# Kernel tuning notes

Hardware: AMD Instinct MI355X
Metric: run time of the kernel (lower is better)

## Reference

```python
import jax, jax.numpy as jnp
import numpy as np

N = 4096        # total nodes per batched graph
E_EDGES = 65536 # edges per graph (avg degree 16)
B = 16          # graphs in batch
NFEAT = 1280
NHID = 512
NHEAD = 8
DFF = 2048      # TransformerEncoderLayer default dim_feedforward
HD = NHID // NHEAD
LN_EPS = 1e-5


def setup_inputs() -> dict:
    key = jax.random.key(0)
    ks = jax.random.split(key, 32)
    s = 0.02
    inp = {}
    inp["fea1"] = jax.random.normal(ks[0], (N, NFEAT), jnp.float32)
    inp["fea2"] = jax.random.normal(ks[1], (N, NFEAT), jnp.float32)
    inp["src1"] = jax.random.randint(ks[2], (E_EDGES,), 0, N, jnp.int32)
    inp["dst1"] = jax.random.randint(ks[3], (E_EDGES,), 0, N, jnp.int32)
    inp["src2"] = jax.random.randint(ks[4], (E_EDGES,), 0, N, jnp.int32)
    inp["dst2"] = jax.random.randint(ks[5], (E_EDGES,), 0, N, jnp.int32)
    seg = ((jnp.arange(N) * B) // N).astype(jnp.int32)  # equal-size graphs, sorted ids
    inp["seg1"] = seg
    inp["seg2"] = seg
    inp["num_graphs"] = B
    # GraphConv params (torch Linear convention: y = x @ W.T + b)
    inp["W1"] = jax.random.normal(ks[6], (NHID, NFEAT), jnp.float32) * s
    inp["b1"] = jnp.zeros((NHID,), jnp.float32)
    inp["W2"] = jax.random.normal(ks[7], (NHID, NHID), jnp.float32) * s
    inp["b2"] = jnp.zeros((NHID,), jnp.float32)
    # TransformerEncoderLayer params
    inp["in_proj_w"] = jax.random.normal(ks[8], (3 * NHID, NHID), jnp.float32) * s
    inp["in_proj_b"] = jnp.zeros((3 * NHID,), jnp.float32)
    inp["out_proj_w"] = jax.random.normal(ks[9], (NHID, NHID), jnp.float32) * s
    inp["out_proj_b"] = jnp.zeros((NHID,), jnp.float32)
    inp["ln1_g"] = jnp.ones((NHID,), jnp.float32)
    inp["ln1_b"] = jnp.zeros((NHID,), jnp.float32)
    inp["ln2_g"] = jnp.ones((NHID,), jnp.float32)
    inp["ln2_b"] = jnp.zeros((NHID,), jnp.float32)
    inp["ff1_w"] = jax.random.normal(ks[10], (DFF, NHID), jnp.float32) * s
    inp["ff1_b"] = jnp.zeros((DFF,), jnp.float32)
    inp["ff2_w"] = jax.random.normal(ks[11], (NHID, DFF), jnp.float32) * s
    inp["ff2_b"] = jnp.zeros((NHID,), jnp.float32)
    # MLP head
    inp["l1_w"] = jax.random.normal(ks[12], (512, NHID), jnp.float32) * s
    inp["l1_b"] = jnp.zeros((512,), jnp.float32)
    inp["l2_w"] = jax.random.normal(ks[13], (128, 512), jnp.float32) * s
    inp["l2_b"] = jnp.zeros((128,), jnp.float32)
    inp["l3_w"] = jax.random.normal(ks[14], (2, 128), jnp.float32) * s
    inp["l3_b"] = jnp.zeros((2,), jnp.float32)
    return inp


def graph_conv(fea, src, dst, W, b):
    # DGL GraphConv, norm='both': D_in^{-1/2} A D_out^{-1/2} X W + b (W applied pre-agg)
    ones = jnp.ones(src.shape[0], fea.dtype)
    deg_out = jnp.maximum(jax.ops.segment_sum(ones, src, num_segments=N), 1.0)
    deg_in = jnp.maximum(jax.ops.segment_sum(ones, dst, num_segments=N), 1.0)
    h = fea * (deg_out ** -0.5)[:, None]
    h = h @ W.T  # [N, nhid]
    agg = jax.ops.segment_sum(h[src], dst, num_segments=N)  # scatter-add over edges
    return agg * (deg_in ** -0.5)[:, None] + b


def layer_norm(x, g, b):
    mu = jnp.mean(x, -1, keepdims=True)
    var = jnp.mean((x - mu) ** 2, -1, keepdims=True)
    return (x - mu) * jax.lax.rsqrt(var + LN_EPS) * g + b


def encoder_layer(x, in_proj_w, in_proj_b, out_proj_w, out_proj_b,
                  ln1_g, ln1_b, ln2_g, ln2_b, ff1_w, ff1_b, ff2_w, ff2_b):
    # post-norm TransformerEncoderLayer, unbatched [S, E] input, eval mode (no dropout)
    qkv = x @ in_proj_w.T + in_proj_b               # [S, 3E]
    q, k, v = jnp.split(qkv, 3, axis=-1)
    S = x.shape[0]
    q = q.reshape(S, NHEAD, HD).transpose(1, 0, 2)  # [H, S, hd]
    k = k.reshape(S, NHEAD, HD).transpose(1, 0, 2)
    v = v.reshape(S, NHEAD, HD).transpose(1, 0, 2)
    scores = jnp.einsum('hqd,hkd->hqk', q, k) / jnp.sqrt(jnp.float32(HD))
    attn = jax.nn.softmax(scores, axis=-1)
    ctx = jnp.einsum('hqk,hkd->hqd', attn, v).transpose(1, 0, 2).reshape(S, NHID)
    x = layer_norm(x + (ctx @ out_proj_w.T + out_proj_b), ln1_g, ln1_b)
    ff = jax.nn.relu(x @ ff1_w.T + ff1_b) @ ff2_w.T + ff2_b
    return layer_norm(x + ff, ln2_g, ln2_b)


def mean_nodes(fea, seg, num_graphs):
    counts = jnp.maximum(jax.ops.segment_sum(jnp.ones(fea.shape[0], fea.dtype), seg, num_segments=num_graphs), 1.0)
    return jax.ops.segment_sum(fea, seg, num_segments=num_graphs) / counts[:, None]


def reference(fea1, fea2, W1, b1, W2, b2, in_proj_w, in_proj_b, out_proj_w, out_proj_b,
              ln1_g, ln1_b, ln2_g, ln2_b, ff1_w, ff1_b, ff2_w, ff2_b,
              l1_w, l1_b, l2_w, l2_b, l3_w, l3_b,
              src1, dst1, src2, dst2, seg1, seg2, num_graphs):
    tparams = (in_proj_w, in_proj_b, out_proj_w, out_proj_b,
               ln1_g, ln1_b, ln2_g, ln2_b, ff1_w, ff1_b, ff2_w, ff2_b)
    h1 = jax.nn.relu(graph_conv(fea1, src1, dst1, W1, b1))
    h2 = jax.nn.relu(graph_conv(fea2, src2, dst2, W1, b1))
    h1 = encoder_layer(h1, *tparams)
    h2 = encoder_layer(h2, *tparams)
    h1 = jax.nn.relu(graph_conv(h1, src1, dst1, W2, b2))
    h2 = jax.nn.relu(graph_conv(h2, src2, dst2, W2, b2))
    hg = mean_nodes(h1, seg1, num_graphs) * mean_nodes(h2, seg2, num_graphs)  # [B, nhid]
    out = hg @ l1_w.T + l1_b          # note: original has NO activation between l1/l2/l3
    out = out @ l2_w.T + l2_b
    return jax.nn.softmax(out @ l3_w.T + l3_b, axis=-1)
```

## Files before the change

kernel.cpp:

```cpp
#include <hip/hip_runtime.h>
#include <hip/hip_bf16.h>
#include <math.h>

#define NN 4096
#define EE 65536
#define NS 8192
#define NFEAT 1280
#define NHID 512
#define DFF 2048

typedef unsigned short u16;
typedef unsigned int u32;
typedef __attribute__((ext_vector_type(8))) short bf16x8;
typedef __attribute__((ext_vector_type(4))) float f32x4;
#define MFMA16(A,B,C) __builtin_amdgcn_mfma_f32_16x16x32_bf16(A,B,C,0,0,0)
#define GAS __attribute__((address_space(1)))
#define LAS __attribute__((address_space(3)))

#define SCL 0.18033688011112042f
#define THR 11.541560327111707f

static const size_t OFF_A   = 0ull;
static const size_t OFF_HP  = 8388608ull;
static const size_t OFF_X   = 12582912ull;
static const size_t OFF_XB  = 16777216ull;
static const size_t OFF_E   = 18874368ull;
static const size_t OFF_VT  = 25165824ull;
static const size_t OFF_CTB = 27262976ull;
static const size_t OFF_W1B = 29360128ull;
static const size_t OFF_IPB = 29687808ull;
static const size_t OFF_OPB = 30081024ull;
static const size_t OFF_F1B = 30212096ull;
static const size_t OFF_F2B = 30736384ull;
static const size_t OFF_W2B = 31260672ull;
static const size_t OFF_ME  = 31391744ull;
static const size_t OFF_DG  = 31408128ull;
static const size_t OFF_INT = 31424512ull;

#define IH_S1 0
#define IH_D1 4096
#define IH_S2 8192
#define IH_D2 12288
#define IO_F1 16384
#define IO_F2 20608
#define IC_1  24832
#define IC_2  28928
#define IE_1  33024
#define IE_2  98560

__device__ __forceinline__ u16 f2b(float x) {
    u32 u = __float_as_uint(x);
    return (u16)((u + 0x7fffu + ((u >> 16) & 1u)) >> 16);
}
__device__ __forceinline__ float b_lo(u32 u) { return __uint_as_float(u << 16); }
__device__ __forceinline__ float b_hi(u32 u) { return __uint_as_float(u & 0xffff0000u); }

__global__ __launch_bounds__(256) void k_hist(const int* __restrict__ s1, const int* __restrict__ d1,
                                              const int* __restrict__ s2, const int* __restrict__ d2,
                                              int* __restrict__ I)
{
    int e = blockIdx.x * 256 + threadIdx.x;
    if (e < EE) {
        atomicAdd(&I[IH_S1 + s1[e]], 1);
        atomicAdd(&I[IH_D1 + d1[e]], 1);
        atomicAdd(&I[IH_S2 + s2[e]], 1);
        atomicAdd(&I[IH_D2 + d2[e]], 1);
    }
}

__global__ __launch_bounds__(256) void k_deg_fin(const int* __restrict__ I, float* __restrict__ deg)
{
    int i = blockIdx.x * 256 + threadIdx.x;
    if (i < 4 * NN) deg[i] = rsqrtf(fmaxf((float)I[i], 1.0f));
}

__global__ __launch_bounds__(256) void k_scan(int* __restrict__ I)
{
    int b = blockIdx.x;
    const int* hist = I + (b ? IH_D2 : IH_D1);
    int* offs = I + (b ? IO_F2 : IO_F1);
    int* cur  = I + (b ? IC_2 : IC_1);
    __shared__ int part[256];
    int t = threadIdx.x;
    int base = t * 16;
    int loc[16];
    int s = 0;
#pragma unroll
    for (int i = 0; i < 16; ++i) { loc[i] = s; s += hist[base + i]; }
    part[t] = s;
    __syncthreads();
    if (t == 0) {
        int a = 0;
        for (int i = 0; i < 256; ++i) { int v = part[i]; part[i] = a; a += v; }
        offs[NN] = a;
    }
    __syncthreads();
    int p = part[t];
#pragma unroll
    for (int i = 0; i < 16; ++i) { offs[base + i] = p + loc[i]; cur[base + i] = p + loc[i]; }
}

__global__ __launch_bounds__(256) void k_fill(const int* __restrict__ s1, const int* __restrict__ d1,
                                              const int* __restrict__ s2, const int* __restrict__ d2,
                                              int* __restrict__ I)
{
    int e = blockIdx.x * 256 + threadIdx.x;
    if (e < EE) {
        int p1 = atomicAdd(&I[IC_1 + d1[e]], 1);
        I[IE_1 + p1] = s1[e];
        int p2 = atomicAdd(&I[IC_2 + d2[e]], 1);
        I[IE_2 + p2] = s2[e];
    }
}

__global__ __launch_bounds__(256) void k_cvt(const float* __restrict__ src, u16* __restrict__ dst, int n)
{
    int i = (blockIdx.x * 256 + threadIdx.x) * 8;
    if (i >= n) return;
    float4 a = *(const float4*)&src[i];
    float4 b = *(const float4*)&src[i + 4];
    uint4 o;
    o.x = (u32)f2b(a.x) | ((u32)f2b(a.y) << 16);
    o.y = (u32)f2b(a.z) | ((u32)f2b(a.w) << 16);
    o.z = (u32)f2b(b.x) | ((u32)f2b(b.y) << 16);
    o.w = (u32)f2b(b.z) | ((u32)f2b(b.w) << 16);
    *(uint4*)&dst[i] = o;
}

__global__ __launch_bounds__(256) void k_scale_bf(const float* __restrict__ in1, const float* __restrict__ in2,
                                                  const float* __restrict__ sc1, const float* __restrict__ sc2,
                                                  u16* __restrict__ out, int ncol)
{
    int quads = ncol >> 2;
    long long idx = (long long)blockIdx.x * 256 + threadIdx.x;
    if (idx >= (long long)NS * quads) return;
    int r  = (int)(idx / quads);
    int cq = (int)(idx % quads) * 4;
    const float* in; const float* sc; int rr;
    if (r < NN) { in = in1; sc = sc1; rr = r; } else { in = in2; sc = sc2; rr = r - NN; }
    float4 v = *(const float4*)&in[(size_t)rr * ncol + cq];
    float s = sc[rr];
    uint2 o;
    o.x = (u32)f2b(v.x * s) | ((u32)f2b(v.y * s) << 16);
    o.y = (u32)f2b(v.z * s) | ((u32)f2b(v.w * s) << 16);
    *(uint2*)&out[(size_t)r * ncol + cq] = o;
}

template<int BN>
__global__ __launch_bounds__(256) void k_gemm_bf(const u16* __restrict__ A, const u16* __restrict__ W,
                                                 const float* __restrict__ bias, float* __restrict__ Cf,
                                                 u16* __restrict__ Cb, int M, int N, int K, int relu)
{
    constexpr int RM = (BN == 128) ? 4 : 2;
    __shared__ u16 As[128 * 32];
    __shared__ u16 Bs[BN * 32];
    int t = threadIdx.x;
    int w = t >> 6, L = t & 63;
    int lm = L & 15, lq = L >> 4;
    int wr = (BN == 128) ? (w >> 1) : w;
    int wc = (BN == 128) ? (w & 1) : 0;
    int row0 = blockIdx.y * 128, col0 = blockIdx.x * BN;
    f32x4 acc[RM][4];
#pragma unroll
    for (int i = 0; i < RM; ++i)
#pragma unroll
        for (int j = 0; j < 4; ++j) acc[i][j] = (f32x4){0.f, 0.f, 0.f, 0.f};

    const u16* As0 = &A[(size_t)(row0 + (w * 2) * 16 + (L >> 2)) * K + (L & 3) * 8];
    const u16* As1 = As0 + (size_t)16 * K;
    const u16* Bs0 = &W[(size_t)(col0 + ((BN == 128) ? (w * 2) * 16 : w * 16) + (L >> 2)) * K + (L & 3) * 8];
    const u16* Bs1 = Bs0 + (size_t)16 * K;
    u16* AsW = &As[(w * 2) * 512];
    u16* BsW = (BN == 128) ? &Bs[(w * 2) * 512] : &Bs[w * 512];

    for (int k0 = 0; k0 < K; k0 += 32) {
        if (k0) __syncthreads();
        __builtin_amdgcn_global_load_lds((const GAS void*)(As0 + k0), (LAS void*)(LAS char*)AsW, 16, 0, 0);
        __builtin_amdgcn_global_load_lds((const GAS void*)(As1 + k0), (LAS void*)((LAS char*)AsW + 1024), 16, 0, 0);
        __builtin_amdgcn_global_load_lds((const GAS void*)(Bs0 + k0), (LAS void*)(LAS char*)BsW, 16, 0, 0);
        if constexpr (BN == 128)
            __builtin_amdgcn_global_load_lds((const GAS void*)(Bs1 + k0), (LAS void*)((LAS char*)BsW + 1024), 16, 0, 0);
        __syncthreads();
        bf16x8 af[RM], bw[4];
#pragma unroll
        for (int i = 0; i < RM; ++i)
            af[i] = *(const bf16x8*)&As[(wr * (RM * 16) + i * 16 + lm) * 32 + lq * 8];
#pragma unroll
        for (int j = 0; j < 4; ++j)
            bw[j] = *(const bf16x8*)&Bs[(wc * 64 + j * 16 + lm) * 32 + lq * 8];
#pragma unroll
        for (int i = 0; i < RM; ++i)
#pragma unroll
            for (int j = 0; j < 4; ++j)
                acc[i][j] = MFMA16(af[i], bw[j], acc[i][j]);
    }

#pragma unroll
    for (int i = 0; i < RM; ++i) {
        int row = row0 + wr * (RM * 16) + i * 16 + lq * 4;
#pragma unroll
        for (int j = 0; j < 4; ++j) {
            int col = col0 + wc * 64 + j * 16 + lm;
            float bv = bias ? bias[col] : 0.0f;
#pragma unroll
            for (int r = 0; r < 4; ++r) {
                float v = acc[i][j][r] + bv;
                if (relu) v = fmaxf(v, 0.0f);
                size_t off = (size_t)(row + r) * N + col;
                if (Cb) Cb[off] = f2b(v);
                else    Cf[off] = v;
            }
        }
    }
}

__global__ __launch_bounds__(256) void k_gather_bf(const u16* __restrict__ hp, const int* __restrict__ I,
                                                   const float* __restrict__ din1, const float* __restrict__ din2,
                                                   const float* __restrict__ bias,
                                                   float* __restrict__ xout, u16* __restrict__ xb)
{
    int r = blockIdx.x, c = threadIdx.x;
    int g = r >> 12, rl = r & (NN - 1);
    const int* off = I + (g ? IO_F2 : IO_F1);
    const int* eid = I + (g ? IE_2 : IE_1);
    int beg = off[rl], end = off[rl + 1];
    const u16* base = hp + ((size_t)g << 12) * NHID;
    float a0 = 0.f, a1 = 0.f;
    for (int i = beg; i < end; ++i) {
        u32 v = ((const u32*)(base + (size_t)eid[i] * NHID))[c];
        a0 += b_lo(v);
        a1 += b_hi(v);
    }
    float s = (g ? din2 : din1)[rl];
    float2 bv = *(const float2*)&bias[c * 2];
    float v0 = fmaxf(fmaf(a0, s, bv.x), 0.f);
    float v1 = fmaxf(fmaf(a1, s, bv.y), 0.f);
    size_t o = (size_t)r * NHID + c * 2;
    if (xout) *(float2*)&xout[o] = make_float2(v0, v1);
    if (xb) *(u32*)&xb[o] = (u32)f2b(v0) | ((u32)f2b(v1) << 16);
}

__global__ __launch_bounds__(256) void k_vtrans(const u16* __restrict__ qkvb, u16* __restrict__ vtb)
{
    __shared__ u16 tile[64][65];
    int t = threadIdx.x;
    int kt = blockIdx.x, h = blockIdx.y, g = blockIdx.z;
    int k0 = kt * 64;
    size_t gbase = (size_t)g * NN;
#pragma unroll
    for (int p = 0; p < 4; ++p) {
        int kl = p * 16 + (t >> 4);
        int d  = (t & 15) * 4;
        uint2 v = *(const uint2*)&qkvb[(gbase + k0 + kl) * 1536 + 1024 + h * 64 + d];
        tile[kl][d + 0] = (u16)(v.x & 0xffff);
        tile[kl][d + 1] = (u16)(v.x >> 16);
        tile[kl][d + 2] = (u16)(v.y & 0xffff);
        tile[kl][d + 3] = (u16)(v.y >> 16);
    }
    __syncthreads();
#pragma unroll
    for (int p = 0; p < 4; ++p) {
        int dl = p * 16 + (t >> 4);
        int kap = (t & 15) * 4;
        u16 v0 = tile[(t & 15) + 0][dl];
        u16 v1 = tile[(t & 15) + 16][dl];
        u16 v2 = tile[(t & 15) + 32][dl];
        u16 v3 = tile[(t & 15) + 48][dl];
        uint2 o;
        o.x = (u32)v0 | ((u32)v1 << 16);
        o.y = (u32)v2 | ((u32)v3 << 16);
        *(uint2*)&vtb[((size_t)(g * 8 + h) * 64 + dl) * (size_t)NN + k0 + kap] = o;
    }
}

__global__ __launch_bounds__(256, 2) void k_attn(const u16* __restrict__ qkv,
                                                 const u16* __restrict__ vt,
                                                 u16* __restrict__ ctb)
{
    __shared__ __align__(16) u16 Kl[2][64 * 64];
    __shared__ __align__(16) u16 Vl[2][64 * 64];
    __shared__ __align__(16) u16 Pl[4][32 * 64];
    int t = threadIdx.x;
    int w = t >> 6, L = t & 63;
    int lm = L & 15, lq = L >> 4;
    int qt = blockIdx.x, h = blockIdx.y, g = blockIdx.z;
    size_t gbase = (size_t)g * NN;
    int q0 = qt * 128 + w * 32;

    const u16* kbase = &qkv[gbase * 1536 + 512 + h * 64];
    const u16* vbase = &vt[(size_t)(g * 8 + h) * 64 * (size_t)NN];

    int srcb = ((L & 7) * 16) ^ ((L >> 3) << 4);
    int rho0 = (w * 2) * 8 + (L >> 3);
    int rho1 = rho0 + 8;
    int kp0 = (rho0 & 15) * 4 + (rho0 >> 4);
    int kp1 = (rho1 & 15) * 4 + (rho1 >> 4);
    const u16* kg0 = &kbase[(size_t)kp0 * 1536 + (srcb >> 1)];
    const u16* kg1 = &kbase[(size_t)kp1 * 1536 + (srcb >> 1)];
    const u16* vg0 = &vbase[(size_t)rho0 * NN + (srcb >> 1)];
    const u16* vg1 = &vbase[(size_t)rho1 * NN + (srcb >> 1)];
    u16* Pw = &Pl[w][0];

    bf16x8 qa[2][2];
#pragma unroll
    for (int qg = 0; qg < 2; ++qg) {
        const u16* qp = &qkv[(gbase + q0 + qg * 16 + lm) * 1536 + h * 64 + lq * 8];
        qa[qg][0] = *(const bf16x8*)qp;
        qa[qg][1] = *(const bf16x8*)(qp + 32);
    }
    f32x4 ctx[2][4];
#pragma unroll
    for (int qg = 0; qg < 2; ++qg)
#pragma unroll
        for (int n = 0; n < 4; ++n) ctx[qg][n] = (f32x4){0.f, 0.f, 0.f, 0.f};
    float m[2][4], lsum[2][4];
#pragma unroll
    for (int qg = 0; qg < 2; ++qg)
#pragma unroll
        for (int r = 0; r < 4; ++r) { m[qg][r] = -1e30f; lsum[qg][r] = 0.0f; }

    __builtin_amdgcn_global_load_lds((const GAS void*)kg0, (LAS void*)((LAS char*)&Kl[0][0] + (w * 2) * 1024), 16, 0, 0);
    __builtin_amdgcn_global_load_lds((const GAS void*)kg1, (LAS void*)((LAS char*)&Kl[0][0] + (w * 2 + 1) * 1024), 16, 0, 0);
    __builtin_amdgcn_global_load_lds((const GAS void*)vg0, (LAS void*)((LAS char*)&Vl[0][0] + (w * 2) * 1024), 16, 0, 0);
    __builtin_amdgcn_global_load_lds((const GAS void*)vg1, (LAS void*)((LAS char*)&Vl[0][0] + (w * 2 + 1) * 1024), 16, 0, 0);
    __syncthreads();

    int cur = 0;
    for (int t0 = 0; t0 < NN; t0 += 64) {
        if (t0 + 64 < NN) {
            size_t ko = (size_t)(t0 + 64) * 1536;
            __builtin_amdgcn_global_load_lds((const GAS void*)(kg0 + ko), (LAS void*)((LAS char*)&Kl[cur ^ 1][0] + (w * 2) * 1024), 16, 0, 0);
            __builtin_amdgcn_global_load_lds((const GAS void*)(kg1 + ko), (LAS void*)((LAS char*)&Kl[cur ^ 1][0] + (w * 2 + 1) * 1024), 16, 0, 0);
            __builtin_amdgcn_global_load_lds((const GAS void*)(vg0 + t0 + 64), (LAS void*)((LAS char*)&Vl[cur ^ 1][0] + (w * 2) * 1024), 16, 0, 0);
            __builtin_amdgcn_global_load_lds((const GAS void*)(vg1 + t0 + 64), (LAS void*)((LAS char*)&Vl[cur ^ 1][0] + (w * 2 + 1) * 1024), 16, 0, 0);
        }
        const char* Kc = (const char*)&Kl[cur][0];
        const char* Vc = (const char*)&Vl[cur][0];
        int sw = (lm & 7) << 4;

        f32x4 s[2][4];
        __builtin_amdgcn_s_setprio(1);
#pragma unroll
        for (int kc = 0; kc < 4; ++kc) {
            const char* rp = Kc + (kc * 16 + lm) * 128;
            bf16x8 kb0 = *(const bf16x8*)(rp + ((lq * 16) ^ sw));
            bf16x8 kb1 = *(const bf16x8*)(rp + ((64 + lq * 16) ^ sw));
#pragma unroll
            for (int qg = 0; qg < 2; ++qg) {
                f32x4 z = (f32x4){0.f, 0.f, 0.f, 0.f};
                z = MFMA16(qa[qg][0], kb0, z);
                z = MFMA16(qa[qg][1], kb1, z);
                s[qg][kc] = z * SCL;
            }
        }
        __builtin_amdgcn_s_setprio(0);

        float dmax = -1e30f;
#pragma unroll
        for (int qg = 0; qg < 2; ++qg)
#pragma unroll
            for (int r = 0; r < 4; ++r) {
                float a = fmaxf(fmaxf(s[qg][0][r], s[qg][1][r]), fmaxf(s[qg][2][r], s[qg][3][r]));
                dmax = fmaxf(dmax, a - m[qg][r]);
            }
        if (__any(dmax > THR)) {
#pragma unroll
            for (int qg = 0; qg < 2; ++qg)
#pragma unroll
                for (int r = 0; r < 4; ++r) {
                    float mr = fmaxf(fmaxf(s[qg][0][r], s[qg][1][r]), fmaxf(s[qg][2][r], s[qg][3][r]));
                    mr = fmaxf(mr, __shfl_xor(mr, 1));
                    mr = fmaxf(mr, __shfl_xor(mr, 2));
                    mr = fmaxf(mr, __shfl_xor(mr, 4));
                    mr = fmaxf(mr, __shfl_xor(mr, 8));
                    float mn = fmaxf(m[qg][r], mr);
                    float corr = exp2f(m[qg][r] - mn);
                    m[qg][r] = mn;
                    lsum[qg][r] *= corr;
#pragma unroll
                    for (int n = 0; n < 4; ++n) ctx[qg][n][r] *= corr;
                }
        }
#pragma unroll
        for (int qg = 0; qg < 2; ++qg)
#pragma unroll
            for (int r = 0; r < 4; ++r) {
                float mq = m[qg][r];
                float p0 = exp2f(s[qg][0][r] - mq);
                float p1 = exp2f(s[qg][1][r] - mq);
                float p2 = exp2f(s[qg][2][r] - mq);
                float p3 = exp2f(s[qg][3][r] - mq);
                lsum[qg][r] += (p0 + p1) + (p2 + p3);
                int row = qg * 16 + lq * 4 + r;
                __hip_bfloat162 c0 = __float22bfloat162_rn(make_float2(p0, p1));
                __hip_bfloat162 c1 = __float22bfloat162_rn(make_float2(p2, p3));
                uint2 pv;
                pv.x = *(u32*)&c0;
                pv.y = *(u32*)&c1;
                *(uint2*)((char*)Pw + row * 128 + ((lm * 8) ^ ((row & 7) << 4))) = pv;
            }

        __builtin_amdgcn_s_setprio(1);
        bf16x8 vbf[4][2];
#pragma unroll
        for (int n = 0; n < 4; ++n) {
            const char* vr = Vc + (n * 16 + lm) * 128;
            vbf[n][0] = *(const bf16x8*)(vr + ((lq * 16) ^ sw));
            vbf[n][1] = *(const bf16x8*)(vr + ((64 + lq * 16) ^ sw));
        }
#pragma unroll
        for (int qg = 0; qg < 2; ++qg) {
            const char* pr = (const char*)Pw + (qg * 16 + lm) * 128;
            bf16x8 pa0 = *(const bf16x8*)(pr + ((lq * 16) ^ sw));
            bf16x8 pa1 = *(const bf16x8*)(pr + ((64 + lq * 16) ^ sw));
#pragma unroll
            for (int n = 0; n < 4; ++n) {
                ctx[qg][n] = MFMA16(pa0, vbf[n][0], ctx[qg][n]);
                ctx[qg][n] = MFMA16(pa1, vbf[n][1], ctx[qg][n]);
            }
        }
        __builtin_amdgcn_s_setprio(0);

        __syncthreads();
        cur ^= 1;
    }

#pragma unroll
    for (int qg = 0; qg < 2; ++qg) {
        float inv[4];
#pragma unroll
        for (int r = 0; r < 4; ++r) {
            float lr = lsum[qg][r];
            lr += __shfl_xor(lr, 1);
            lr += __shfl_xor(lr, 2);
            lr += __shfl_xor(lr, 4);
            lr += __shfl_xor(lr, 8);
            inv[r] = 1.0f / lr;
        }
#pragma unroll
        for (int n = 0; n < 4; ++n)
#pragma unroll
            for (int r = 0; r < 4; ++r) {
                int row = q0 + qg * 16 + lq * 4 + r;
                int col = h * 64 + n * 16 + lm;
                ctb[(gbase + row) * NHID + col] = f2b(ctx[qg][n][r] * inv[r]);
            }
    }
}

__global__ __launch_bounds__(256) void k_add_ln(const float* __restrict__ x, const float* __restrict__ y,
                                                const float* __restrict__ g, const float* __restrict__ bb,
                                                float* __restrict__ xout, u16* __restrict__ xb,
                                                const float* __restrict__ sc1, const float* __restrict__ sc2)
{
    int r = blockIdx.x, tid = threadIdx.x;
    int c = tid * 2;
    float2 xv = *(const float2*)&x[(size_t)r * NHID + c];
    float2 yv = *(const float2*)&y[(size_t)r * NHID + c];
    float a0 = xv.x + yv.x, a1 = xv.y + yv.y;
    float s = a0 + a1;
    float qs = a0 * a0 + a1 * a1;
#pragma unroll
    for (int off = 32; off > 0; off >>= 1) {
        s  += __shfl_xor(s, off);
        qs += __shfl_xor(qs, off);
    }
    __shared__ float ss[4], qq[4];
    int w = tid >> 6;
    if ((tid & 63) == 0) { ss[w] = s; qq[w] = qs; }
    __syncthreads();
    s  = ss[0] + ss[1] + ss[2] + ss[3];
    qs = qq[0] + qq[1] + qq[2] + qq[3];
    float mu  = s * (1.0f / NHID);
    float var = qs * (1.0f / NHID) - mu * mu;
    float rs = rsqrtf(var + 1e-5f);
    float2 gv = *(const float2*)&g[c];
    float2 bv = *(const float2*)&bb[c];
    float o0 = (a0 - mu) * rs * gv.x + bv.x;
    float o1 = (a1 - mu) * rs * gv.y + bv.y;
    if (xout) *(float2*)&xout[(size_t)r * NHID + c] = make_float2(o0, o1);
    float sc = 1.0f;
    if (sc1) sc = (r < NN) ? sc1[r] : sc2[r - NN];
    u32 o = (u32)f2b(o0 * sc) | ((u32)f2b(o1 * sc) << 16);
    *(u32*)&xb[(size_t)r * NHID + c] = o;
}

__global__ __launch_bounds__(512) void k_seg_mean(const float* __restrict__ h, float* __restrict__ means)
{
    int b = blockIdx.x;
    int st = blockIdx.y;
    int col = threadIdx.x;
    const float* hp = &h[((size_t)st * NN + (size_t)b * 256) * NHID + col];
    float acc = 0.0f;
    for (int i = 0; i < 256; ++i) acc += hp[(size_t)i * NHID];
    means[((size_t)st * 16 + b) * NHID + col] = acc * (1.0f / 256.0f);
}

__global__ __launch_bounds__(256) void k_head(const float* __restrict__ means,
                                              const float* __restrict__ l1w, const float* __restrict__ l1b,
                                              const float* __restrict__ l2w, const float* __restrict__ l2b,
                                              const float* __restrict__ l3w, const float* __restrict__ l3b,
                                              float* __restrict__ out)
{
    __shared__ float hg[512];
    __shared__ float t1[512];
    __shared__ float t2[128];
    int b = blockIdx.x;
    int t = threadIdx.x;
    hg[t]       = means[b * 512 + t]       * means[(16 + b) * 512 + t];
    hg[t + 256] = means[b * 512 + t + 256] * means[(16 + b) * 512 + t + 256];
    __syncthreads();
#pragma unroll
    for (int o = t; o < 512; o += 256) {
        const float* wr = &l1w[(size_t)o * 512];
        float acc = l1b[o];
        for (int k = 0; k < 512; k += 4) {
            float4 w = *(const float4*)&wr[k];
            acc = fmaf(hg[k], w.x, acc);
            acc = fmaf(hg[k + 1], w.y, acc);
            acc = fmaf(hg[k + 2], w.z, acc);
            acc = fmaf(hg[k + 3], w.w, acc);
        }
        t1[o] = acc;
    }
    __syncthreads();
    if (t < 128) {
        const float* wr = &l2w[(size_t)t * 512];
        float acc = l2b[t];
        for (int k = 0; k < 512; k += 4) {
            float4 w = *(const float4*)&wr[k];
            acc = fmaf(t1[k], w.x, acc);
            acc = fmaf(t1[k + 1], w.y, acc);
            acc = fmaf(t1[k + 2], w.z, acc);
            acc = fmaf(t1[k + 3], w.w, acc);
        }
        t2[t] = acc;
    }
    __syncthreads();
    if (t < 64) {
        float p0 = t2[t] * l3w[t] + t2[t + 64] * l3w[t + 64];
        float p1 = t2[t] * l3w[128 + t] + t2[t + 64] * l3w[128 + t + 64];
#pragma unroll
        for (int off = 32; off > 0; off >>= 1) {
            p0 += __shfl_xor(p0, off);
            p1 += __shfl_xor(p1, off);
        }
        if (t == 0) {
            float v0 = p0 + l3b[0], v1 = p1 + l3b[1];
            float mx = fmaxf(v0, v1);
            float e0 = __expf(v0 - mx), e1 = __expf(v1 - mx);
            float inv = 1.0f / (e0 + e1);
            out[b * 2 + 0] = e0 * inv;
            out[b * 2 + 1] = e1 * inv;
        }
    }
}

extern "C" void kernel_launch(void* const* d_in, const int* in_sizes, int n_in,
                              void* d_out, int out_size, void* d_ws, size_t ws_size,
                              hipStream_t stream)
{
    const float* fea1 = (const float*)d_in[0];
    const float* fea2 = (const float*)d_in[1];
    const int* src1 = (const int*)d_in[2];
    const int* dst1 = (const int*)d_in[3];
    const int* src2 = (const int*)d_in[4];
    const int* dst2 = (const int*)d_in[5];
    const float* W1 = (const float*)d_in[9];
    const float* b1 = (const float*)d_in[10];
    const float* W2 = (const float*)d_in[11];
    const float* b2 = (const float*)d_in[12];
    const float* in_proj_w = (const float*)d_in[13];
    const float* in_proj_b = (const float*)d_in[14];
    const float* out_proj_w = (const float*)d_in[15];
    const float* out_proj_b = (const float*)d_in[16];
    const float* ln1_g = (const float*)d_in[17];
    const float* ln1_b = (const float*)d_in[18];
    const float* ln2_g = (const float*)d_in[19];
    const float* ln2_b = (const float*)d_in[20];
    const float* ff1_w = (const float*)d_in[21];
    const float* ff1_b = (const float*)d_in[22];
    const float* ff2_w = (const float*)d_in[23];
    const float* ff2_b = (const float*)d_in[24];
    const float* l1_w = (const float*)d_in[25];
    const float* l1_b = (const float*)d_in[26];
    const float* l2_w = (const float*)d_in[27];
    const float* l2_b = (const float*)d_in[28];
    const float* l3_w = (const float*)d_in[29];
    const float* l3_b = (const float*)d_in[30];

    float* ws = (float*)d_ws;
    u16*  Ab   = (u16*)(ws + OFF_A);
    float* HP  = ws + OFF_HP;
    u16*  HPb  = (u16*)(ws + OFF_HP);
    float* X   = ws + OFF_X;
    u16*  Xb   = (u16*)(ws + OFF_XB);
    u16*  QKVb = (u16*)(ws + OFF_E);
    float* AG2 = ws + OFF_E;
    u16*  Vtb  = (u16*)(ws + OFF_VT);
    u16*  CTb  = (u16*)(ws + OFF_CTB);
    u16*  W1b  = (u16*)(ws + OFF_W1B);
    u16*  IPb  = (u16*)(ws + OFF_IPB);
    u16*  OPb  = (u16*)(ws + OFF_OPB);
    u16*  F1b  = (u16*)(ws + OFF_F1B);
    u16*  F2b  = (u16*)(ws + OFF_F2B);
    u16*  W2b  = (u16*)(ws + OFF_W2B);
    float* ME  = ws + OFF_ME;
    float* DG  = ws + OFF_DG;
    int*   I   = (int*)(ws + OFF_INT);
    float* dout1 = DG;
    float* din1  = DG + NN;
    float* dout2 = DG + 2 * NN;
    float* din2  = DG + 3 * NN;

    hipMemsetAsync(I, 0, 4 * NN * sizeof(int), stream);

    k_hist<<<EE / 256, 256, 0, stream>>>(src1, dst1, src2, dst2, I);
    k_deg_fin<<<(4 * NN) / 256, 256, 0, stream>>>(I, DG);
    k_scan<<<2, 256, 0, stream>>>(I);
    k_fill<<<EE / 256, 256, 0, stream>>>(src1, dst1, src2, dst2, I);

    k_cvt<<<(NHID * NFEAT / 8 + 255) / 256, 256, 0, stream>>>(W1, W1b, NHID * NFEAT);
    k_cvt<<<(3 * NHID * NHID / 8 + 255) / 256, 256, 0, stream>>>(in_proj_w, IPb, 3 * NHID * NHID);
    k_cvt<<<(NHID * NHID / 8 + 255) / 256, 256, 0, stream>>>(out_proj_w, OPb, NHID * NHID);
    k_cvt<<<(DFF * NHID / 8 + 255) / 256, 256, 0, stream>>>(ff1_w, F1b, DFF * NHID);
    k_cvt<<<(NHID * DFF / 8 + 255) / 256, 256, 0, stream>>>(ff2_w, F2b, NHID * DFF);
    k_cvt<<<(NHID * NHID / 8 + 255) / 256, 256, 0, stream>>>(W2, W2b, NHID * NHID);

    {
        long long tq = (long long)NS * (NFEAT / 4);
        k_scale_bf<<<(int)((tq + 255) / 256), 256, 0, stream>>>(fea1, fea2, dout1, dout2, Ab, NFEAT);
    }
    k_gemm_bf<64><<<dim3(NHID / 64, NS / 128), 256, 0, stream>>>(Ab, W1b, nullptr, nullptr, HPb, NS, NHID, NFEAT, 0);
    k_gather_bf<<<NS, 256, 0, stream>>>(HPb, I, din1, din2, b1, X, Xb);

    k_gemm_bf<128><<<dim3(1536 / 128, NS / 128), 256, 0, stream>>>(Xb, IPb, in_proj_b, nullptr, QKVb, NS, 1536, NHID, 0);
    k_vtrans<<<dim3(NN / 64, 8, 2), 256, 0, stream>>>(QKVb, Vtb);
    k_attn<<<dim3(NN / 128, 8, 2), 256, 0, stream>>>(QKVb, Vtb, CTb);
    k_gemm_bf<64><<<dim3(NHID / 64, NS / 128), 256, 0, stream>>>(CTb, OPb, out_proj_b, HP, nullptr, NS, NHID, NHID, 0);
    k_add_ln<<<NS, 256, 0, stream>>>(X, HP, ln1_g, ln1_b, X, Xb, nullptr, nullptr);
    k_gemm_bf<128><<<dim3(DFF / 128, NS / 128), 256, 0, stream>>>(Xb, F1b, ff1_b, nullptr, Ab, NS, DFF, NHID, 1);
    k_gemm_bf<64><<<dim3(NHID / 64, NS / 128), 256, 0, stream>>>(Ab, F2b, ff2_b, HP, nullptr, NS, NHID, DFF, 0);
    k_add_ln<<<NS, 256, 0, stream>>>(X, HP, ln2_g, ln2_b, nullptr, Ab, dout1, dout2);

    k_gemm_bf<64><<<dim3(NHID / 64, NS / 128), 256, 0, stream>>>(Ab, W2b, nullptr, nullptr, HPb, NS, NHID, NHID, 0);
    k_gather_bf<<<NS, 256, 0, stream>>>(HPb, I, din1, din2, b2, AG2, nullptr);

    k_seg_mean<<<dim3(16, 2), 512, 0, stream>>>(AG2, ME);
    k_head<<<16, 256, 0, stream>>>(ME, l1_w, l1_b, l2_w, l2_b, l3_w, l3_b, (float*)d_out);
}
```

Measured before the change: 628.8 us.

## Halve attention query tile per wave and fold softmax scale into QKV GEMM

The attention kernel now gives each wave 16 query rows instead of 32, halving the per-block query tile and the P scratch buffer, and raises the launch-bounds occupancy hint from 2 to 4 blocks per CU. Register and LDS pressure drops and more waves can be resident, but each K/V tile loaded into LDS is now reused by half as many queries, which doubles K/V traffic. The softmax scale multiply is moved out of the inner attention loop into the QKV GEMM epilogue, applied only to the Q columns. This removes a per-score multiply at the cost of one extra scale in the GEMM epilogue.

```diff
diff --git a/kernel.cpp b/kernel.cpp
--- a/kernel.cpp
+++ b/kernel.cpp
@@ -149,7 +149,8 @@
 template<int BN>
 __global__ __launch_bounds__(256) void k_gemm_bf(const u16* __restrict__ A, const u16* __restrict__ W,
                                                  const float* __restrict__ bias, float* __restrict__ Cf,
-                                                 u16* __restrict__ Cb, int M, int N, int K, int relu)
+                                                 u16* __restrict__ Cb, int M, int N, int K, int relu,
+                                                 int qcols)
 {
     constexpr int RM = (BN == 128) ? 4 : 2;
     __shared__ u16 As[128 * 32];
@@ -202,10 +203,12 @@
         for (int j = 0; j < 4; ++j) {
             int col = col0 + wc * 64 + j * 16 + lm;
             float bv = bias ? bias[col] : 0.0f;
+            float cs = (col < qcols) ? SCL : 1.0f;
 #pragma unroll
             for (int r = 0; r < 4; ++r) {
                 float v = acc[i][j][r] + bv;
                 if (relu) v = fmaxf(v, 0.0f);
+                v *= cs;
                 size_t off = (size_t)(row + r) * N + col;
                 if (Cb) Cb[off] = f2b(v);
                 else    Cf[off] = v;
@@ -273,19 +276,19 @@
     }
 }
 
-__global__ __launch_bounds__(256, 2) void k_attn(const u16* __restrict__ qkv,
+__global__ __launch_bounds__(256, 4) void k_attn(const u16* __restrict__ qkv,
                                                  const u16* __restrict__ vt,
                                                  u16* __restrict__ ctb)
 {
     __shared__ __align__(16) u16 Kl[2][64 * 64];
     __shared__ __align__(16) u16 Vl[2][64 * 64];
-    __shared__ __align__(16) u16 Pl[4][32 * 64];
+    __shared__ __align__(16) u16 Pl[4][16 * 64];
     int t = threadIdx.x;
     int w = t >> 6, L = t & 63;
     int lm = L & 15, lq = L >> 4;
     int qt = blockIdx.x, h = blockIdx.y, g = blockIdx.z;
     size_t gbase = (size_t)g * NN;
-    int q0 = qt * 128 + w * 32;
+    int q0 = qt * 64 + w * 16;
 
     const u16* kbase = &qkv[gbase * 1536 + 512 + h * 64];
     const u16* vbase = &vt[(size_t)(g * 8 + h) * 64 * (size_t)NN];
@@ -301,23 +304,16 @@
     const u16* vg1 = &vbase[(size_t)rho1 * NN + (srcb >> 1)];
     u16* Pw = &Pl[w][0];
 
-    bf16x8 qa[2][2];
-#pragma unroll
-    for (int qg = 0; qg < 2; ++qg) {
-        const u16* qp = &qkv[(gbase + q0 + qg * 16 + lm) * 1536 + h * 64 + lq * 8];
-        qa[qg][0] = *(const bf16x8*)qp;
-        qa[qg][1] = *(const bf16x8*)(qp + 32);
-    }
-    f32x4 ctx[2][4];
-#pragma unroll
-    for (int qg = 0; qg < 2; ++qg)
-#pragma unroll
-        for (int n = 0; n < 4; ++n) ctx[qg][n] = (f32x4){0.f, 0.f, 0.f, 0.f};
-    float m[2][4], lsum[2][4];
-#pragma unroll
-    for (int qg = 0; qg < 2; ++qg)
-#pragma unroll
-        for (int r = 0; r < 4; ++r) { m[qg][r] = -1e30f; lsum[qg][r] = 0.0f; }
+    const u16* qp = &qkv[(gbase + q0 + lm) * 1536 + h * 64 + lq * 8];
+    bf16x8 qa0 = *(const bf16x8*)qp;
+    bf16x8 qa1 = *(const bf16x8*)(qp + 32);
+
+    f32x4 ctx[4];
+#pragma unroll
+    for (int n = 0; n < 4; ++n) ctx[n] = (f32x4){0.f, 0.f, 0.f, 0.f};
+    float m[4], lsum[4];
+#pragma unroll
+    for (int r = 0; r < 4; ++r) { m[r] = -1e30f; lsum[r] = 0.0f; }
 
     __builtin_amdgcn_global_load_lds((const GAS void*)kg0, (LAS void*)((LAS char*)&Kl[0][0] + (w * 2) * 1024), 16, 0, 0);
     __builtin_amdgcn_global_load_lds((const GAS void*)kg1, (LAS void*)((LAS char*)&Kl[0][0] + (w * 2 + 1) * 1024), 16, 0, 0);
@@ -338,85 +334,71 @@
         const char* Vc = (const char*)&Vl[cur][0];
         int sw = (lm & 7) << 4;
 
-        f32x4 s[2][4];
+        f32x4 s[4];
         __builtin_amdgcn_s_setprio(1);
 #pragma unroll
         for (int kc = 0; kc < 4; ++kc) {
             const char* rp = Kc + (kc * 16 + lm) * 128;
             bf16x8 kb0 = *(const bf16x8*)(rp + ((lq * 16) ^ sw));
             bf16x8 kb1 = *(const bf16x8*)(rp + ((64 + lq * 16) ^ sw));
-#pragma unroll
-            for (int qg = 0; qg < 2; ++qg) {
-                f32x4 z = (f32x4){0.f, 0.f, 0.f, 0.f};
-                z = MFMA16(qa[qg][0], kb0, z);
-                z = MFMA16(qa[qg][1], kb1, z);
-                s[qg][kc] = z * SCL;
+            f32x4 z = (f32x4){0.f, 0.f, 0.f, 0.f};
+            z = MFMA16(qa0, kb0, z);
+            z = MFMA16(qa1, kb1, z);
+            s[kc] = z;
+        }
+        __builtin_amdgcn_s_setprio(0);
+
+        float dmax = -1e30f;
+#pragma unroll
+        for (int r = 0; r < 4; ++r) {
+            float a = fmaxf(fmaxf(s[0][r], s[1][r]), fmaxf(s[2][r], s[3][r]));
+            dmax = fmaxf(dmax, a - m[r]);
+        }
+        if (__any(dmax > THR)) {
+#pragma unroll
+            for (int r = 0; r < 4; ++r) {
+                float mr = fmaxf(fmaxf(s[0][r], s[1][r]), fmaxf(s[2][r], s[3][r]));
+                mr = fmaxf(mr, __shfl_xor(mr, 1));
+                mr = fmaxf(mr, __shfl_xor(mr, 2));
+                mr = fmaxf(mr, __shfl_xor(mr, 4));
+                mr = fmaxf(mr, __shfl_xor(mr, 8));
+                float mn = fmaxf(m[r], mr);
+                float corr = exp2f(m[r] - mn);
+                m[r] = mn;
+                lsum[r] *= corr;
+#pragma unroll
+                for (int n = 0; n < 4; ++n) ctx[n][r] *= corr;
             }
         }
-        __builtin_amdgcn_s_setprio(0);
-
-        float dmax = -1e30f;
-#pragma unroll
-        for (int qg = 0; qg < 2; ++qg)
-#pragma unroll
-            for (int r = 0; r < 4; ++r) {
-                float a = fmaxf(fmaxf(s[qg][0][r], s[qg][1][r]), fmaxf(s[qg][2][r], s[qg][3][r]));
-                dmax = fmaxf(dmax, a - m[qg][r]);
-            }
-        if (__any(dmax > THR)) {
-#pragma unroll
-            for (int qg = 0; qg < 2; ++qg)
-#pragma unroll
-                for (int r = 0; r < 4; ++r) {
-                    float mr = fmaxf(fmaxf(s[qg][0][r], s[qg][1][r]), fmaxf(s[qg][2][r], s[qg][3][r]));
-                    mr = fmaxf(mr, __shfl_xor(mr, 1));
-                    mr = fmaxf(mr, __shfl_xor(mr, 2));
-                    mr = fmaxf(mr, __shfl_xor(mr, 4));
-                    mr = fmaxf(mr, __shfl_xor(mr, 8));
-                    float mn = fmaxf(m[qg][r], mr);
-                    float corr = exp2f(m[qg][r] - mn);
-                    m[qg][r] = mn;
-                    lsum[qg][r] *= corr;
-#pragma unroll
-                    for (int n = 0; n < 4; ++n) ctx[qg][n][r] *= corr;
-                }
-        }
-#pragma unroll
-        for (int qg = 0; qg < 2; ++qg)
-#pragma unroll
-            for (int r = 0; r < 4; ++r) {
-                float mq = m[qg][r];
-                float p0 = exp2f(s[qg][0][r] - mq);
-                float p1 = exp2f(s[qg][1][r] - mq);
-                float p2 = exp2f(s[qg][2][r] - mq);
-                float p3 = exp2f(s[qg][3][r] - mq);
-                lsum[qg][r] += (p0 + p1) + (p2 + p3);
-                int row = qg * 16 + lq * 4 + r;
-                __hip_bfloat162 c0 = __float22bfloat162_rn(make_float2(p0, p1));
-                __hip_bfloat162 c1 = __float22bfloat162_rn(make_float2(p2, p3));
-                uint2 pv;
-                pv.x = *(u32*)&c0;
-                pv.y = *(u32*)&c1;
-                *(uint2*)((char*)Pw + row * 128 + ((lm * 8) ^ ((row & 7) << 4))) = pv;
-            }
+#pragma unroll
+        for (int r = 0; r < 4; ++r) {
+            float mq = m[r];
+            float p0 = exp2f(s[0][r] - mq);
+            float p1 = exp2f(s[1][r] - mq);
+            float p2 = exp2f(s[2][r] - mq);
+            float p3 = exp2f(s[3][r] - mq);
+            lsum[r] += (p0 + p1) + (p2 + p3);
+            int row = lq * 4 + r;
+            __hip_bfloat162 c0 = __float22bfloat162_rn(make_float2(p0, p1));
+            __hip_bfloat162 c1 = __float22bfloat162_rn(make_float2(p2, p3));
+            uint2 pv;
+            pv.x = *(u32*)&c0;
+            pv.y = *(u32*)&c1;
+            *(uint2*)((char*)Pw + row * 128 + ((lm * 8) ^ ((row & 7) << 4))) = pv;
+        }
 
         __builtin_amdgcn_s_setprio(1);
-        bf16x8 vbf[4][2];
-#pragma unroll
-        for (int n = 0; n < 4; ++n) {
-            const char* vr = Vc + (n * 16 + lm) * 128;
-            vbf[n][0] = *(const bf16x8*)(vr + ((lq * 16) ^ sw));
-            vbf[n][1] = *(const bf16x8*)(vr + ((64 + lq * 16) ^ sw));
-        }
-#pragma unroll
-        for (int qg = 0; qg < 2; ++qg) {
-            const char* pr = (const char*)Pw + (qg * 16 + lm) * 128;
+        {
+            const char* pr = (const char*)Pw + lm * 128;
             bf16x8 pa0 = *(const bf16x8*)(pr + ((lq * 16) ^ sw));
             bf16x8 pa1 = *(const bf16x8*)(pr + ((64 + lq * 16) ^ sw));
 #pragma unroll
             for (int n = 0; n < 4; ++n) {
-                ctx[qg][n] = MFMA16(pa0, vbf[n][0], ctx[qg][n]);
-                ctx[qg][n] = MFMA16(pa1, vbf[n][1], ctx[qg][n]);
+                const char* vr = Vc + (n * 16 + lm) * 128;
+                bf16x8 vb0 = *(const bf16x8*)(vr + ((lq * 16) ^ sw));
+                bf16x8 vb1 = *(const bf16x8*)(vr + ((64 + lq * 16) ^ sw));
+                ctx[n] = MFMA16(pa0, vb0, ctx[n]);
+                ctx[n] = MFMA16(pa1, vb1, ctx[n]);
             }
         }
         __builtin_amdgcn_s_setprio(0);
@@ -425,27 +407,24 @@
         cur ^= 1;
     }
 
-#pragma unroll
-    for (int qg = 0; qg < 2; ++qg) {
-        float inv[4];
+    float inv[4];
+#pragma unroll
+    for (int r = 0; r < 4; ++r) {
+        float lr = lsum[r];
+        lr += __shfl_xor(lr, 1);
+        lr += __shfl_xor(lr, 2);
+        lr += __shfl_xor(lr, 4);
+        lr += __shfl_xor(lr, 8);
+        inv[r] = 1.0f / lr;
+    }
+#pragma unroll
+    for (int n = 0; n < 4; ++n)
 #pragma unroll
         for (int r = 0; r < 4; ++r) {
-            float lr = lsum[qg][r];
-            lr += __shfl_xor(lr, 1);
-            lr += __shfl_xor(lr, 2);
-            lr += __shfl_xor(lr, 4);
-            lr += __shfl_xor(lr, 8);
-            inv[r] = 1.0f / lr;
-        }
-#pragma unroll
-        for (int n = 0; n < 4; ++n)
-#pragma unroll
-            for (int r = 0; r < 4; ++r) {
-                int row = q0 + qg * 16 + lq * 4 + r;
-                int col = h * 64 + n * 16 + lm;
-                ctb[(gbase + row) * NHID + col] = f2b(ctx[qg][n][r] * inv[r]);
-            }
-    }
+            int row = q0 + lq * 4 + r;
+            int col = h * 64 + n * 16 + lm;
+            ctb[(gbase + row) * NHID + col] = f2b(ctx[n][r] * inv[r]);
+        }
 }
 
 __global__ __launch_bounds__(256) void k_add_ln(const float* __restrict__ x, const float* __restrict__ y,
@@ -631,19 +610,19 @@
         long long tq = (long long)NS * (NFEAT / 4);
         k_scale_bf<<<(int)((tq + 255) / 256), 256, 0, stream>>>(fea1, fea2, dout1, dout2, Ab, NFEAT);
     }
-    k_gemm_bf<64><<<dim3(NHID / 64, NS / 128), 256, 0, stream>>>(Ab, W1b, nullptr, nullptr, HPb, NS, NHID, NFEAT, 0);
+    k_gemm_bf<64><<<dim3(NHID / 64, NS / 128), 256, 0, stream>>>(Ab, W1b, nullptr, nullptr, HPb, NS, NHID, NFEAT, 0, 0);
     k_gather_bf<<<NS, 256, 0, stream>>>(HPb, I, din1, din2, b1, X, Xb);
 
-    k_gemm_bf<128><<<dim3(1536 / 128, NS / 128), 256, 0, stream>>>(Xb, IPb, in_proj_b, nullptr, QKVb, NS, 1536, NHID, 0);
+    k_gemm_bf<128><<<dim3(1536 / 128, NS / 128), 256, 0, stream>>>(Xb, IPb, in_proj_b, nullptr, QKVb, NS, 1536, NHID, 0, NHID);
     k_vtrans<<<dim3(NN / 64, 8, 2), 256, 0, stream>>>(QKVb, Vtb);
-    k_attn<<<dim3(NN / 128, 8, 2), 256, 0, stream>>>(QKVb, Vtb, CTb);
-    k_gemm_bf<64><<<dim3(NHID / 64, NS / 128), 256, 0, stream>>>(CTb, OPb, out_proj_b, HP, nullptr, NS, NHID, NHID, 0);
+    k_attn<<<dim3(NN / 64, 8, 2), 256, 0, stream>>>(QKVb, Vtb, CTb);
+    k_gemm_bf<64><<<dim3(NHID / 64, NS / 128), 256, 0, stream>>>(CTb, OPb, out_proj_b, HP, nullptr, NS, NHID, NHID, 0, 0);
     k_add_ln<<<NS, 256, 0, stream>>>(X, HP, ln1_g, ln1_b, X, Xb, nullptr, nullptr);
-    k_gemm_bf<128><<<dim3(DFF / 128, NS / 128), 256, 0, stream>>>(Xb, F1b, ff1_b, nullptr, Ab, NS, DFF, NHID, 1);
-    k_gemm_bf<64><<<dim3(NHID / 64, NS / 128), 256, 0, stream>>>(Ab, F2b, ff2_b, HP, nullptr, NS, NHID, DFF, 0);
+    k_gemm_bf<128><<<dim3(DFF / 128, NS / 128), 256, 0, stream>>>(Xb, F1b, ff1_b, nullptr, Ab, NS, DFF, NHID, 1, 0);
+    k_gemm_bf<64><<<dim3(NHID / 64, NS / 128), 256, 0, stream>>>(Ab, F2b, ff2_b, HP, nullptr, NS, NHID, DFF, 0, 0);
     k_add_ln<<<NS, 256, 0, stream>>>(X, HP, ln2_g, ln2_b, nullptr, Ab, dout1, dout2);
 
-    k_gemm_bf<64><<<dim3(NHID / 64, NS / 128), 256, 0, stream>>>(Ab, W2b, nullptr, nullptr, HPb, NS, NHID, NHID, 0);
+    k_gemm_bf<64><<<dim3(NHID / 64, NS / 128), 256, 0, stream>>>(Ab, W2b, nullptr, nullptr, HPb, NS, NHID, NHID, 0, 0);
     k_gather_bf<<<NS, 256, 0, stream>>>(HPb, I, din1, din2, b2, AG2, nullptr);
 
     k_seg_mean<<<dim3(16, 2), 512, 0, stream>>>(AG2, ME);
```

Result: no change. 631.1 us (+0.4%).
